# Kernel tuning notes

Hardware: AMD Instinct MI355X
Metric: run time of the kernel (lower is better)

The kernel has to match this reference:

```python
import jax, jax.numpy as jnp
import numpy as np

OBS = 64      # observation_dim = numel of one frame (1*8*8)
EXTRA = 20    # extra_hidden_dim
HID = OBS + EXTRA  # 84
T = 64        # sequence length
B = 16        # batch
L2 = 1e-3     # l2_regularization


def setup_inputs() -> dict:
    key = jax.random.key(0)
    k1, k2, k3 = jax.random.split(key, 3)
    # xavier_uniform-style init for A and C
    A = jax.random.uniform(k1, (HID, HID), minval=-1.0, maxval=1.0) * np.sqrt(6.0 / (HID + HID))
    C = jax.random.uniform(k2, (OBS, HID), minval=-1.0, maxval=1.0) * np.sqrt(6.0 / (OBS + HID))
    x = jax.random.normal(k3, (B, T, 1, 8, 8), dtype=jnp.float32)
    return {"x": x, "A": A.astype(jnp.float32), "C": C.astype(jnp.float32), "step": 0}


def build_M(A, C, seq_len):
    # T_reg = C with l2 added on its leading 'diagonal' entries C[k,k]
    d = jnp.arange(OBS)
    Treg = C.at[d, d].add(L2)
    # blocks[k] = Treg @ A^k, computed by a single scan (no Python loop over T^2)
    def step(carry, _):
        return carry @ A, carry
    _, blocks = jax.lax.scan(step, Treg, None, length=seq_len)  # [T, OBS, HID]
    i = jnp.arange(seq_len)
    diff = i[:, None] - i[None, :]                               # block (i,j) -> A-power i-j
    Mb = jnp.where((diff >= 0)[:, :, None, None],
                   blocks[jnp.clip(diff, 0, seq_len - 1)], 0.0)  # [T, T, OBS, HID]
    # block layout -> dense [T*OBS, T*HID]
    return Mb.transpose(0, 2, 1, 3).reshape(seq_len * OBS, seq_len * HID)


def reference(x, A, C, step):
    Bsz, seq_len = x.shape[0], x.shape[1]
    M = build_M(A, C, seq_len)                   # [T*OBS, T*HID]
    MMT = M @ M.T                                # [T*OBS, T*OBS]
    U = jnp.linalg.cholesky(MMT)                 # lower, as torch.potrf(upper=False)
    # The flow is an external invertible network; surrogate: identity flow, loss = 0
    zcat = x.reshape(Bsz, -1)                    # [B, T*OBS]
    Y = zcat
    z = jax.scipy.linalg.solve_triangular(U, Y.T, lower=True)          # U z = Y^T
    z = jax.scipy.linalg.solve_triangular(U, z, lower=True, trans='T')  # U^T z = z
    xe = (M.T @ z).T                             # [B, T*HID]
    eps = xe[:, HID:]                            # drop first hidden block
    prediction_loss = jnp.mean(eps * eps)        # + flow loss (0 for identity surrogate)
    return prediction_loss
```

## Files before the change

kernel.cpp:

```cpp
#include <hip/hip_runtime.h>

#define OBS 64
#define EXT 20
#define HID 84
#define TT  64
#define BB  16

#define OFF_T1INV 0
#define OFF_XT    4096
#define OFF_NA1   5376
#define OFF_ANT1  6656
#define OFF_ANA1  7936
#define OFF_N     9216
#define OFF_AN    10896
#define OFF_D     12576
#define OFF_DLAST 12976
#define OFF_F     13376
#define OFF_Q     13776
#define OFF_G     79312
#define OFF_JG    99792
#define OFF_ZG    125392
#define OFF_TS    150992
#define OFF_PART  171472
#define OFF_ICONV OFF_D

#define RDLANE(v, l) __uint_as_float(__builtin_amdgcn_readlane((int)__float_as_uint(v), (l)))

__device__ __forceinline__ void ld20(const float* p, float a[20]) {
    const float4* q = (const float4*)p;
    float4 v0 = q[0], v1 = q[1], v2 = q[2], v3 = q[3], v4 = q[4];
    a[0]=v0.x; a[1]=v0.y; a[2]=v0.z; a[3]=v0.w;
    a[4]=v1.x; a[5]=v1.y; a[6]=v1.z; a[7]=v1.w;
    a[8]=v2.x; a[9]=v2.y; a[10]=v2.z; a[11]=v2.w;
    a[12]=v3.x; a[13]=v3.y; a[14]=v3.z; a[15]=v3.w;
    a[16]=v4.x; a[17]=v4.y; a[18]=v4.z; a[19]=v4.w;
}

__device__ __forceinline__ float dot20(const float a[20], const float v[20]) {
    float s0 = 0.f, s1 = 0.f, s2 = 0.f, s3 = 0.f;
    #pragma unroll
    for (int m = 0; m < 20; m += 4) {
        s0 += a[m]     * v[m];
        s1 += a[m + 1] * v[m + 1];
        s2 += a[m + 2] * v[m + 2];
        s3 += a[m + 3] * v[m + 3];
    }
    return (s0 + s1) + (s2 + s3);
}

__device__ __forceinline__ void gj32_split(int lane, float w[32],
                                           float* __restrict__ sOut) {
    int r = lane & 31;
    bool mat = (lane < 32);
    bool used = false; int myk = 0;
    #pragma unroll
    for (int k = 0; k < 32; ++k) {
        float ak = __shfl(w[k], r);
        float v = (mat && !used) ? fabsf(ak) : -1.0f;
        int idx = r;
        #pragma unroll
        for (int off = 32; off; off >>= 1) {
            float v2 = __shfl_down(v, off);
            int   i2 = __shfl_down(idx, off);
            if (v2 > v) { v = v2; idx = i2; }
        }
        int p = __shfl(idx, 0);
        float piv = RDLANE(w[k], p);
        float rp  = 1.0f / piv;
        bool isp  = (r == p);
        float coeff = isp ? rp : -(ak * rp);
        if (mat && isp) { used = true; myk = k; }
        int psrc = p | (lane & 32);
        #pragma unroll
        for (int c = 0; c < 32; ++c) {
            float prc = __shfl(w[c], psrc);
            w[c] = isp ? (prc * rp) : fmaf(prc, coeff, w[c]);
        }
    }
    int myk2 = __shfl(myk, r);
    if (!mat) {
        #pragma unroll
        for (int c = 0; c < 32; ++c) sOut[myk2 * 32 + c] = w[c];
    }
}

__global__ __launch_bounds__(512) void k_prep(const float* __restrict__ A,
                                              const float* __restrict__ C,
                                              float* __restrict__ ws) {
    __shared__ float sPinv[1024], sW[1024], sV[1024], sSc[1024];
    __shared__ float sScinv[1024], sX1[1024], sX2[1024];
    __shared__ float Xs[64][20];
    __shared__ float Ns[84][20];
    __shared__ float ANs[84][20];
    int tid = threadIdx.x, wave = tid >> 6, lane = tid & 63;

    if (wave == 0) {
        int r = lane & 31;
        float w[32];
        #pragma unroll
        for (int c = 0; c < 32; ++c)
            w[c] = (lane < 32) ? (C[r * HID + c] + (c == r ? 1e-3f : 0.0f))
                               : ((c == r) ? 1.0f : 0.0f);
        gj32_split(lane, w, sPinv);
    }
    __syncthreads();

    for (int id = tid; id < 2048; id += 512) {
        int sel = id >> 10, rc = id & 1023, r = rc >> 5, c = rc & 31;
        float s = 0.f;
        if (sel == 0) {
            for (int m = 0; m < 32; ++m) s += C[(32 + r) * HID + m] * sPinv[m * 32 + c];
            sW[rc] = s;
        } else {
            for (int m = 0; m < 32; ++m) s += sPinv[r * 32 + m] * C[m * HID + 32 + c];
            sV[rc] = s;
        }
    }
    __syncthreads();

    for (int id = tid; id < 1024; id += 512) {
        int r = id >> 5, c = id & 31;
        float s = C[(32 + r) * HID + 32 + c] + (r == c ? 1e-3f : 0.f);
        for (int m = 0; m < 32; ++m) s -= sW[r * 32 + m] * C[m * HID + 32 + c];
        sSc[id] = s;
    }
    __syncthreads();

    if (wave == 0) {
        int r = lane & 31;
        float w[32];
        #pragma unroll
        for (int c = 0; c < 32; ++c)
            w[c] = (lane < 32) ? sSc[r * 32 + c] : ((c == r) ? 1.0f : 0.0f);
        gj32_split(lane, w, sScinv);
    }
    __syncthreads();

    for (int id = tid; id < 2048; id += 512) {
        int sel = id >> 10, rc = id & 1023, r = rc >> 5, c = rc & 31;
        float s = 0.f;
        if (sel == 0) {
            for (int m = 0; m < 32; ++m) s += sScinv[r * 32 + m] * sW[m * 32 + c];
            sX1[rc] = s;
        } else {
            for (int m = 0; m < 32; ++m) s += sV[r * 32 + m] * sScinv[m * 32 + c];
            sX2[rc] = s;
        }
    }
    __syncthreads();

    for (int id = tid; id < 1024; id += 512) {
        int r = id >> 5, c = id & 31;
        float x3 = 0.f;
        for (int m = 0; m < 32; ++m) x3 += sV[r * 32 + m] * sX1[m * 32 + c];
        ws[OFF_T1INV + r * 64 + c]              = sPinv[id] + x3;
        ws[OFF_T1INV + r * 64 + 32 + c]         = -sX2[id];
        ws[OFF_T1INV + (32 + r) * 64 + c]       = -sX1[id];
        ws[OFF_T1INV + (32 + r) * 64 + 32 + c]  = sScinv[id];
    }
    __syncthreads();

    for (int id = tid; id < 64 * 20; id += 512) {
        int r = id / 20, j = id % 20;
        float s = 0.f;
        const float* tr = ws + OFF_T1INV + r * 64;
        for (int c = 0; c < 64; ++c) s += tr[c] * C[c * HID + 64 + j];
        Xs[r][j] = s;
        ws[OFF_XT + j * 64 + r] = s;
    }
    __syncthreads();
    for (int id = tid; id < HID * 20; id += 512) {
        int p = id / 20, j = id % 20;
        float v = (p < 64) ? -Xs[p][j] : ((p - 64) == j ? 1.f : 0.f);
        Ns[p][j] = v;
        ws[OFF_N + id] = v;
    }
    __syncthreads();
    for (int id = tid; id < HID * 20; id += 512) {
        int p = id / 20, j = id % 20;
        float s = 0.f;
        for (int m = 0; m < HID; ++m) s += A[p * HID + m] * Ns[m][j];
        ANs[p][j] = s;
        ws[OFF_AN + id] = s;
    }
    __syncthreads();
    for (int id = tid; id < 400; id += 512) {
        int a = id / 20, b = id % 20;
        float sn = 0.f, sf = 0.f, sg = 0.f;
        for (int p = 0; p < HID; ++p) {
            sn += Ns[p][a] * Ns[p][b];
            sf += Ns[p][a] * ANs[p][b];
            sg += ANs[p][a] * ANs[p][b];
        }
        ws[OFF_F + id]     = sf;
        ws[OFF_D + id]     = sn + sg;
        ws[OFF_DLAST + id] = sn;
    }
    for (int id = tid; id < 20 * 64; id += 512) {
        int j = id / 64, c = id % 64;
        float s1 = 0.f, s2 = 0.f;
        for (int p = 0; p < HID; ++p) {
            float av = A[p * HID + c];
            s1 += Ns[p][j] * av;
            s2 += ANs[p][j] * av;
        }
        ws[OFF_NA1 + id]  = s1;
        ws[OFF_ANA1 + id] = s2;
        ws[OFF_ANT1 + id] = ANs[c][j];
    }
}

__global__ __launch_bounds__(64, 1) void k_factor(float* __restrict__ ws) {
    __shared__ float sD[400], sDl[400], sF[400];
    int lane = threadIdx.x;
    for (int id = lane; id < 400; id += 64) {
        sD[id]  = ws[OFF_D + id];
        sDl[id] = ws[OFF_DLAST + id];
        sF[id]  = ws[OFF_F + id];
    }
    __syncthreads();

    float* Jg = ws + OFF_JG;
    float* Zg = ws + OFF_ZG;

    float Kprev[20];
    #pragma unroll
    for (int r = 0; r < 20; ++r) Kprev[r] = 0.f;
    int iconv = 62;
    for (int i = 0; i < 64; ++i) {
        bool last = (i == 63);
        float w[40];
        #pragma unroll
        for (int r = 0; r < 20; ++r) {
            float v, v2 = 0.f;
            if (lane < 20) {
                float dv = last ? sDl[r * 20 + lane] : sD[r * 20 + lane];
                v  = dv - Kprev[r];
                v2 = sF[r * 20 + lane];
            } else if (lane < 40) {
                v = sF[(lane - 20) * 20 + r];
            } else if (lane < 60) {
                v = (r == lane - 40) ? 1.f : 0.f;
            } else {
                v = 0.f;
            }
            w[r]      = v;
            w[20 + r] = v2;
        }
        #pragma unroll
        for (int k = 0; k < 20; ++k) {
            float rp = __builtin_amdgcn_rcpf(RDLANE(w[k], k));
            w[k] *= rp;
            #pragma unroll
            for (int r = 0; r < 40; ++r) {
                if (r == k) continue;
                float ck = RDLANE(w[r], k);
                w[r] -= ck * w[k];
            }
        }
        if (lane >= 40 && lane < 60) {
            int c = lane - 40;
            #pragma unroll
            for (int r = 0; r < 20; ++r) {
                Jg[i * 400 + r * 20 + c] = w[r];
                if (!last) Zg[i * 400 + c * 20 + r] = -w[20 + r];
            }
        }
        if (last) break;
        float dmax = 0.f, kmax = 0.f;
        int gsel = (20 + lane) << 2;
        #pragma unroll
        for (int r = 0; r < 20; ++r) {
            float kn = -__uint_as_float(__builtin_amdgcn_ds_bpermute(
                gsel, (int)__float_as_uint(w[20 + r])));
            dmax = fmaxf(dmax, fabsf(kn - Kprev[r]));
            kmax = fmaxf(kmax, fabsf(kn));
            Kprev[r] = kn;
        }
        if (i < 62 && __all((lane >= 20) || (dmax <= 1e-7f + 1e-4f * kmax))) {
            iconv = i;
            i = 62;
        }
    }
    if (lane == 0) ws[OFF_ICONV] = __int_as_float(iconv);
}

__global__ __launch_bounds__(64) void k_qg(const float* __restrict__ x,
                                           float* __restrict__ ws) {
    int i = blockIdx.x, b = blockIdx.y, r = threadIdx.x;
    __shared__ float yv[3][64];
    __shared__ float qs[3][64];
    yv[1][r] = x[(b * TT + i) * 64 + r];
    yv[0][r] = (i > 0)  ? x[(b * TT + i - 1) * 64 + r] : 0.f;
    yv[2][r] = (i < 63) ? x[(b * TT + i + 1) * 64 + r] : 0.f;
    __syncthreads();
    const float* Ti = ws + OFF_T1INV + r * 64;
    float q0 = 0.f, q1 = 0.f, q2 = 0.f;
    for (int c = 0; c < 64; ++c) {
        float t = Ti[c];
        q0 += t * yv[0][c];
        q1 += t * yv[1][c];
        q2 += t * yv[2][c];
    }
    qs[0][r] = q0; qs[1][r] = q1; qs[2][r] = q2;
    ws[OFF_Q + (b * TT + i) * 64 + r] = q1;
    __syncthreads();
    if (r < 20) {
        const float* xt = ws + OFF_XT   + r * 64;
        const float* na = ws + OFF_NA1  + r * 64;
        const float* at = ws + OFF_ANT1 + r * 64;
        const float* aa = ws + OFF_ANA1 + r * 64;
        float s = 0.f;
        if (i < 63) {
            for (int c = 0; c < 64; ++c)
                s += xt[c] * qs[1][c] + na[c] * qs[0][c] + at[c] * qs[2][c] - aa[c] * qs[1][c];
        } else {
            for (int c = 0; c < 64; ++c)
                s += xt[c] * qs[1][c] + na[c] * qs[0][c];
        }
        ws[OFF_G + (i * 16 + b) * 20 + r] = s;
    }
}

__global__ __launch_bounds__(64, 1) void k_sweeps(float* __restrict__ ws) {
    __shared__ float rh[TT][2][20];
    __shared__ float th[2][20];
    int lane = threadIdx.x;
    int bh   = lane >> 5;
    int b    = (blockIdx.x << 1) + bh;
    int j    = lane & 31;
    int jj   = (j < 20) ? j : 0;
    bool actj = (j < 20);

    int icv = __float_as_int(ws[OFF_ICONV]);
    const float* G  = ws + OFF_G;
    const float* Jg = ws + OFF_JG;
    const float* Zg = ws + OFF_ZG;
    float* TS = ws + OFF_TS;

    float Mrow[20];
    #pragma unroll
    for (int m = 0; m < 20; ++m) Mrow[m] = Zg[icv * 400 + m * 20 + jj];
    float Jr[20], Zr[20], J63r[20];
    ld20(Jg + icv * 400 + jj * 20, Jr);
    ld20(Zg + icv * 400 + jj * 20, Zr);
    ld20(Jg + 63 * 400 + jj * 20, J63r);

    float rt = 0.f, gnext = 0.f;
    if (actj) {
        rt    = G[(0 * 16 + b) * 20 + j];
        rh[0][bh][j] = rt;
        gnext = G[(1 * 16 + b) * 20 + j];
    }
    for (int i = 1; i < TT; ++i) {
        float rv[20];
        ld20(&rh[i - 1][bh][0], rv);
        float s;
        if (i - 1 < icv) {
            float fr[20];
            #pragma unroll
            for (int m = 0; m < 20; ++m) fr[m] = Zg[(i - 1) * 400 + m * 20 + jj];
            s = gnext + dot20(fr, rv);
        } else {
            s = gnext + dot20(Mrow, rv);
        }
        rt = s;
        if (actj) {
            rh[i][bh][j] = rt;
            gnext = (i + 1 < TT) ? G[((i + 1) * 16 + b) * 20 + j] : 0.f;
        }
    }

    {
        float rv[20];
        ld20(&rh[63][bh][0], rv);
        float tn = dot20(J63r, rv);
        if (actj) {
            TS[(63 * 16 + b) * 20 + j] = tn;
            th[bh][j] = tn;
        }
        for (int i = 62; i >= 0; --i) {
            float rvi[20], tv[20];
            ld20(&rh[i][bh][0], rvi);
            ld20(&th[bh][0], tv);
            float t;
            if (i < icv) {
                float jr[20], zr[20];
                ld20(Jg + i * 400 + jj * 20, jr);
                ld20(Zg + i * 400 + jj * 20, zr);
                t = dot20(jr, rvi) + dot20(zr, tv);
            } else {
                t = dot20(Jr, rvi) + dot20(Zr, tv);
            }
            if (actj) {
                TS[(i * 16 + b) * 20 + j] = t;
                th[bh][j] = t;
            }
        }
    }
}

__global__ __launch_bounds__(128) void k_loss(const float* __restrict__ A,
                                              float* __restrict__ ws) {
    int i = blockIdx.x + 1, b = blockIdx.y, tid = threadIdx.x;
    __shared__ float ti[20], tm[20], qi[64], qm[64];
    __shared__ float red[128];
    if (tid < 20) {
        ti[tid] = ws[OFF_TS + (i * 16 + b) * 20 + tid];
        tm[tid] = ws[OFF_TS + ((i - 1) * 16 + b) * 20 + tid];
    }
    if (tid < 64) {
        qi[tid] = ws[OFF_Q + (b * TT + i) * 64 + tid];
        qm[tid] = ws[OFF_Q + (b * TT + i - 1) * 64 + tid];
    }
    __syncthreads();
    float e = 0.f;
    if (tid < HID) {
        int p = tid;
        float s = (p < 64) ? qi[p] : 0.f;
        const float* Np  = ws + OFF_N  + p * 20;
        const float* ANp = ws + OFF_AN + p * 20;
        for (int j = 0; j < 20; ++j) s += Np[j] * ti[j] - ANp[j] * tm[j];
        const float* Ar = A + p * HID;
        for (int c = 0; c < 64; ++c) s -= Ar[c] * qm[c];
        e = s * s;
    }
    red[tid] = e;
    __syncthreads();
    for (int off = 64; off; off >>= 1) {
        if (tid < off) red[tid] += red[tid + off];
        __syncthreads();
    }
    if (tid == 0) ws[OFF_PART + b * 63 + (i - 1)] = red[0];
}

__global__ __launch_bounds__(256) void k_reduce(const float* __restrict__ ws,
                                                float* __restrict__ out) {
    __shared__ float red[256];
    int tid = threadIdx.x;
    float s = 0.f;
    for (int id = tid; id < BB * 63; id += 256) s += ws[OFF_PART + id];
    red[tid] = s;
    __syncthreads();
    for (int off = 128; off; off >>= 1) {
        if (tid < off) red[tid] += red[tid + off];
        __syncthreads();
    }
    if (tid == 0) out[0] = red[0] / (float)(BB * (TT - 1) * HID);
}

extern "C" void kernel_launch(void* const* d_in, const int* in_sizes, int n_in,
                              void* d_out, int out_size, void* d_ws, size_t ws_size,
                              hipStream_t stream) {
    (void)in_sizes; (void)n_in; (void)out_size; (void)ws_size;
    const float* x = (const float*)d_in[0];
    const float* A = (const float*)d_in[1];
    const float* C = (const float*)d_in[2];
    float* ws  = (float*)d_ws;
    float* out = (float*)d_out;

    k_prep  <<<dim3(1),          dim3(512), 0, stream>>>(A, C, ws);
    k_factor<<<dim3(1),          dim3(64),  0, stream>>>(ws);
    k_qg    <<<dim3(TT, BB),     dim3(64),  0, stream>>>(x, ws);
    k_sweeps<<<dim3(8),          dim3(64),  0, stream>>>(ws);
    k_loss  <<<dim3(TT - 1, BB), dim3(128), 0, stream>>>(A, ws);
    k_reduce<<<dim3(1),          dim3(256), 0, stream>>>(ws, out);
}
```

Measured before the change: 189.0 us.

## Fuse factorization into prep and loss into sweep kernel, cutting launches

Moves the block-tridiagonal factorization into the prep kernel, where wave 0 runs it on data kept in shared memory. It also merges the per-timestep loss computation into the sweep kernel, which keeps the solved T vectors in shared memory instead of global memory. This reduces the launch count from six to four and drops several global round-trips. The cost is that the loss work now runs on only 8 single-wave blocks instead of a 63x16 grid, and the other prep waves sit idle during the serial factorization.

```diff
diff --git a/kernel.cpp b/kernel.cpp
--- a/kernel.cpp
+++ b/kernel.cpp
@@ -13,16 +13,12 @@
 #define OFF_ANA1  7936
 #define OFF_N     9216
 #define OFF_AN    10896
-#define OFF_D     12576
-#define OFF_DLAST 12976
-#define OFF_F     13376
+#define OFF_ICONV 12576
 #define OFF_Q     13776
 #define OFF_G     79312
 #define OFF_JG    99792
 #define OFF_ZG    125392
-#define OFF_TS    150992
 #define OFF_PART  171472
-#define OFF_ICONV OFF_D
 
 #define RDLANE(v, l) __uint_as_float(__builtin_amdgcn_readlane((int)__float_as_uint(v), (l)))
 
@@ -92,6 +88,7 @@
     __shared__ float Xs[64][20];
     __shared__ float Ns[84][20];
     __shared__ float ANs[84][20];
+    __shared__ float sD[400], sDl[400], sF[400];
     int tid = threadIdx.x, wave = tid >> 6, lane = tid & 63;
 
     if (wave == 0) {
@@ -192,9 +189,9 @@
             sf += Ns[p][a] * ANs[p][b];
             sg += ANs[p][a] * ANs[p][b];
         }
-        ws[OFF_F + id]     = sf;
-        ws[OFF_D + id]     = sn + sg;
-        ws[OFF_DLAST + id] = sn;
+        sF[id]  = sf;
+        sD[id]  = sn + sg;
+        sDl[id] = sn;
     }
     for (int id = tid; id < 20 * 64; id += 512) {
         int j = id / 64, c = id % 64;
@@ -208,81 +205,72 @@
         ws[OFF_ANA1 + id] = s2;
         ws[OFF_ANT1 + id] = ANs[c][j];
     }
-}
-
-__global__ __launch_bounds__(64, 1) void k_factor(float* __restrict__ ws) {
-    __shared__ float sD[400], sDl[400], sF[400];
-    int lane = threadIdx.x;
-    for (int id = lane; id < 400; id += 64) {
-        sD[id]  = ws[OFF_D + id];
-        sDl[id] = ws[OFF_DLAST + id];
-        sF[id]  = ws[OFF_F + id];
-    }
-    __syncthreads();
-
-    float* Jg = ws + OFF_JG;
-    float* Zg = ws + OFF_ZG;
-
-    float Kprev[20];
-    #pragma unroll
-    for (int r = 0; r < 20; ++r) Kprev[r] = 0.f;
-    int iconv = 62;
-    for (int i = 0; i < 64; ++i) {
-        bool last = (i == 63);
-        float w[40];
-        #pragma unroll
-        for (int r = 0; r < 20; ++r) {
-            float v, v2 = 0.f;
-            if (lane < 20) {
-                float dv = last ? sDl[r * 20 + lane] : sD[r * 20 + lane];
-                v  = dv - Kprev[r];
-                v2 = sF[r * 20 + lane];
-            } else if (lane < 40) {
-                v = sF[(lane - 20) * 20 + r];
-            } else if (lane < 60) {
-                v = (r == lane - 40) ? 1.f : 0.f;
-            } else {
-                v = 0.f;
-            }
-            w[r]      = v;
-            w[20 + r] = v2;
-        }
-        #pragma unroll
-        for (int k = 0; k < 20; ++k) {
-            float rp = __builtin_amdgcn_rcpf(RDLANE(w[k], k));
-            w[k] *= rp;
-            #pragma unroll
-            for (int r = 0; r < 40; ++r) {
-                if (r == k) continue;
-                float ck = RDLANE(w[r], k);
-                w[r] -= ck * w[k];
-            }
-        }
-        if (lane >= 40 && lane < 60) {
-            int c = lane - 40;
+    __syncthreads();
+
+    if (wave == 0) {
+        float* Jg = ws + OFF_JG;
+        float* Zg = ws + OFF_ZG;
+        float Kprev[20];
+        #pragma unroll
+        for (int r = 0; r < 20; ++r) Kprev[r] = 0.f;
+        int iconv = 62;
+        for (int i = 0; i < 64; ++i) {
+            bool last = (i == 63);
+            float w[40];
             #pragma unroll
             for (int r = 0; r < 20; ++r) {
-                Jg[i * 400 + r * 20 + c] = w[r];
-                if (!last) Zg[i * 400 + c * 20 + r] = -w[20 + r];
-            }
-        }
-        if (last) break;
-        float dmax = 0.f, kmax = 0.f;
-        int gsel = (20 + lane) << 2;
-        #pragma unroll
-        for (int r = 0; r < 20; ++r) {
-            float kn = -__uint_as_float(__builtin_amdgcn_ds_bpermute(
-                gsel, (int)__float_as_uint(w[20 + r])));
-            dmax = fmaxf(dmax, fabsf(kn - Kprev[r]));
-            kmax = fmaxf(kmax, fabsf(kn));
-            Kprev[r] = kn;
-        }
-        if (i < 62 && __all((lane >= 20) || (dmax <= 1e-7f + 1e-4f * kmax))) {
-            iconv = i;
-            i = 62;
-        }
-    }
-    if (lane == 0) ws[OFF_ICONV] = __int_as_float(iconv);
+                float v, v2 = 0.f;
+                if (lane < 20) {
+                    float dv = last ? sDl[r * 20 + lane] : sD[r * 20 + lane];
+                    v  = dv - Kprev[r];
+                    v2 = sF[r * 20 + lane];
+                } else if (lane < 40) {
+                    v = sF[(lane - 20) * 20 + r];
+                } else if (lane < 60) {
+                    v = (r == lane - 40) ? 1.f : 0.f;
+                } else {
+                    v = 0.f;
+                }
+                w[r]      = v;
+                w[20 + r] = v2;
+            }
+            #pragma unroll
+            for (int k = 0; k < 20; ++k) {
+                float rp = __builtin_amdgcn_rcpf(RDLANE(w[k], k));
+                w[k] *= rp;
+                #pragma unroll
+                for (int r = 0; r < 40; ++r) {
+                    if (r == k) continue;
+                    float ck = RDLANE(w[r], k);
+                    w[r] -= ck * w[k];
+                }
+            }
+            if (lane >= 40 && lane < 60) {
+                int c = lane - 40;
+                #pragma unroll
+                for (int r = 0; r < 20; ++r) {
+                    Jg[i * 400 + r * 20 + c] = w[r];
+                    if (!last) Zg[i * 400 + c * 20 + r] = -w[20 + r];
+                }
+            }
+            if (last) break;
+            float dmax = 0.f, kmax = 0.f;
+            int gsel = (20 + lane) << 2;
+            #pragma unroll
+            for (int r = 0; r < 20; ++r) {
+                float kn = -__uint_as_float(__builtin_amdgcn_ds_bpermute(
+                    gsel, (int)__float_as_uint(w[20 + r])));
+                dmax = fmaxf(dmax, fabsf(kn - Kprev[r]));
+                kmax = fmaxf(kmax, fabsf(kn));
+                Kprev[r] = kn;
+            }
+            if (i < 62 && __all((lane >= 20) || (dmax <= 1e-7f + 1e-4f * kmax))) {
+                iconv = i;
+                i = 62;
+            }
+        }
+        if (lane == 0) ws[OFF_ICONV] = __int_as_float(iconv);
+    }
 }
 
 __global__ __launch_bounds__(64) void k_qg(const float* __restrict__ x,
@@ -322,21 +310,34 @@
     }
 }
 
-__global__ __launch_bounds__(64, 1) void k_sweeps(float* __restrict__ ws) {
+__global__ __launch_bounds__(64, 1) void k_final(const float* __restrict__ A,
+                                                 const float* __restrict__ x,
+                                                 float* __restrict__ ws) {
     __shared__ float rh[TT][2][20];
-    __shared__ float th[2][20];
+    __shared__ float tsh[TT][2][20];
+    __shared__ float sN[1680], sAN[1680], sA1[5376];
+    __shared__ float qb[2][2][64];
     int lane = threadIdx.x;
     int bh   = lane >> 5;
     int b    = (blockIdx.x << 1) + bh;
     int j    = lane & 31;
     int jj   = (j < 20) ? j : 0;
     bool actj = (j < 20);
+    (void)x;
+
+    for (int id = lane; id < 1680; id += 64) {
+        sN[id]  = ws[OFF_N + id];
+        sAN[id] = ws[OFF_AN + id];
+    }
+    for (int id = lane; id < 5376; id += 64) {
+        int p = id >> 6, c = id & 63;
+        sA1[id] = A[p * HID + c];
+    }
 
     int icv = __float_as_int(ws[OFF_ICONV]);
     const float* G  = ws + OFF_G;
     const float* Jg = ws + OFF_JG;
     const float* Zg = ws + OFF_ZG;
-    float* TS = ws + OFF_TS;
 
     float Mrow[20];
     #pragma unroll
@@ -375,14 +376,11 @@
         float rv[20];
         ld20(&rh[63][bh][0], rv);
         float tn = dot20(J63r, rv);
-        if (actj) {
-            TS[(63 * 16 + b) * 20 + j] = tn;
-            th[bh][j] = tn;
-        }
+        if (actj) tsh[63][bh][j] = tn;
         for (int i = 62; i >= 0; --i) {
             float rvi[20], tv[20];
             ld20(&rh[i][bh][0], rvi);
-            ld20(&th[bh][0], tv);
+            ld20(&tsh[i + 1][bh][0], tv);
             float t;
             if (i < icv) {
                 float jr[20], zr[20];
@@ -392,61 +390,52 @@
             } else {
                 t = dot20(Jr, rvi) + dot20(Zr, tv);
             }
-            if (actj) {
-                TS[(i * 16 + b) * 20 + j] = t;
-                th[bh][j] = t;
-            }
-        }
-    }
-}
-
-__global__ __launch_bounds__(128) void k_loss(const float* __restrict__ A,
-                                              float* __restrict__ ws) {
-    int i = blockIdx.x + 1, b = blockIdx.y, tid = threadIdx.x;
-    __shared__ float ti[20], tm[20], qi[64], qm[64];
-    __shared__ float red[128];
-    if (tid < 20) {
-        ti[tid] = ws[OFF_TS + (i * 16 + b) * 20 + tid];
-        tm[tid] = ws[OFF_TS + ((i - 1) * 16 + b) * 20 + tid];
-    }
-    if (tid < 64) {
-        qi[tid] = ws[OFF_Q + (b * TT + i) * 64 + tid];
-        qm[tid] = ws[OFF_Q + (b * TT + i - 1) * 64 + tid];
-    }
-    __syncthreads();
-    float e = 0.f;
-    if (tid < HID) {
-        int p = tid;
-        float s = (p < 64) ? qi[p] : 0.f;
-        const float* Np  = ws + OFF_N  + p * 20;
-        const float* ANp = ws + OFF_AN + p * 20;
-        for (int j = 0; j < 20; ++j) s += Np[j] * ti[j] - ANp[j] * tm[j];
-        const float* Ar = A + p * HID;
-        for (int c = 0; c < 64; ++c) s -= Ar[c] * qm[c];
-        e = s * s;
-    }
-    red[tid] = e;
-    __syncthreads();
-    for (int off = 64; off; off >>= 1) {
-        if (tid < off) red[tid] += red[tid + off];
-        __syncthreads();
-    }
-    if (tid == 0) ws[OFF_PART + b * 63 + (i - 1)] = red[0];
-}
-
-__global__ __launch_bounds__(256) void k_reduce(const float* __restrict__ ws,
-                                                float* __restrict__ out) {
-    __shared__ float red[256];
-    int tid = threadIdx.x;
-    float s = 0.f;
-    for (int id = tid; id < BB * 63; id += 256) s += ws[OFF_PART + id];
-    red[tid] = s;
-    __syncthreads();
-    for (int off = 128; off; off >>= 1) {
-        if (tid < off) red[tid] += red[tid + off];
-        __syncthreads();
-    }
-    if (tid == 0) out[0] = red[0] / (float)(BB * (TT - 1) * HID);
+            if (actj) tsh[i][bh][j] = t;
+        }
+    }
+
+    const float* Q = ws + OFF_Q;
+    for (int id = lane; id < 128; id += 64) {
+        int s = id >> 6, c = id & 63;
+        qb[0][s][c] = Q[(((blockIdx.x << 1) + s) * TT + 0) * 64 + c];
+    }
+    float acc = 0.f;
+    for (int i = 1; i < TT; ++i) {
+        int cur = i & 1;
+        for (int id = lane; id < 128; id += 64) {
+            int s = id >> 6, c = id & 63;
+            qb[cur][s][c] = Q[(((blockIdx.x << 1) + s) * TT + i) * 64 + c];
+        }
+        #pragma unroll
+        for (int pass = 0; pass < 3; ++pass) {
+            int idx = pass * 64 + lane;
+            if (idx < 168) {
+                int g2 = (idx >= 84) ? 1 : 0;
+                int p  = idx - 84 * g2;
+                float e = (p < 64) ? qb[cur][g2][p] : 0.f;
+                const float* Np  = sN  + p * 20;
+                const float* ANp = sAN + p * 20;
+                for (int jx = 0; jx < 20; ++jx)
+                    e += Np[jx] * tsh[i][g2][jx] - ANp[jx] * tsh[i - 1][g2][jx];
+                const float* Ar = sA1 + p * 64;
+                const float* qm = &qb[cur ^ 1][g2][0];
+                for (int c = 0; c < 64; ++c) e -= Ar[c] * qm[c];
+                acc += e * e;
+            }
+        }
+    }
+    #pragma unroll
+    for (int off = 32; off; off >>= 1) acc += __shfl_down(acc, off);
+    if (lane == 0) ws[OFF_PART + blockIdx.x] = acc;
+}
+
+__global__ __launch_bounds__(64) void k_reduce(const float* __restrict__ ws,
+                                               float* __restrict__ out) {
+    int lane = threadIdx.x;
+    float s = (lane < 8) ? ws[OFF_PART + lane] : 0.f;
+    #pragma unroll
+    for (int off = 8; off; off >>= 1) s += __shfl_down(s, off);
+    if (lane == 0) out[0] = s / (float)(BB * (TT - 1) * HID);
 }
 
 extern "C" void kernel_launch(void* const* d_in, const int* in_sizes, int n_in,
@@ -459,10 +448,8 @@
     float* ws  = (float*)d_ws;
     float* out = (float*)d_out;
 
-    k_prep  <<<dim3(1),          dim3(512), 0, stream>>>(A, C, ws);
-    k_factor<<<dim3(1),          dim3(64),  0, stream>>>(ws);
-    k_qg    <<<dim3(TT, BB),     dim3(64),  0, stream>>>(x, ws);
-    k_sweeps<<<dim3(8),          dim3(64),  0, stream>>>(ws);
-    k_loss  <<<dim3(TT - 1, BB), dim3(128), 0, stream>>>(A, ws);
-    k_reduce<<<dim3(1),          dim3(256), 0, stream>>>(ws, out);
-}
+    k_prep  <<<dim3(1),      dim3(512), 0, stream>>>(A, C, ws);
+    k_qg    <<<dim3(TT, BB), dim3(64),  0, stream>>>(x, ws);
+    k_final <<<dim3(8),      dim3(64),  0, stream>>>(A, x, ws);
+    k_reduce<<<dim3(1),      dim3(64),  0, stream>>>(ws, out);
+}
```

After: 378.2 us. +100.1%, slower.
